# Kernel tuning notes

Hardware: AMD Instinct MI355X
Metric: run time of the kernel (lower is better)

The kernel has to match this reference:

```python
import jax, jax.numpy as jnp
import numpy as np

D_MODEL = 2048
B, L = 4, 2048


def _dwconv(x, w, b):
    # x: (B, D, L), w: (D, 1, 3), b: (D,). Causal depthwise conv (PyTorch pad=2 then [...,:L]).
    y = jax.lax.conv_general_dilated(
        x, w, window_strides=(1,), padding=[(2, 0)],
        feature_group_count=x.shape[1], dimension_numbers=("NCH", "OIH", "NCH"))
    return y + b[None, :, None]


def setup_inputs() -> dict:
    key = jax.random.key(0)
    ks = jax.random.split(key, 12)
    D = D_MODEL
    s = 0.02
    inp = {
        "u": jax.random.normal(ks[0], (B, L, D), jnp.float32),
        "Wq": jax.random.normal(ks[1], (D, D), jnp.float32) * s,
        "bq": jnp.zeros((D,), jnp.float32),
        "Wk": jax.random.normal(ks[2], (D, D), jnp.float32) * s,
        "bk": jnp.zeros((D,), jnp.float32),
        "Wv": jax.random.normal(ks[3], (D, D), jnp.float32) * s,
        "bv": jnp.zeros((D,), jnp.float32),
        "convq_w": jax.random.normal(ks[4], (D, 1, 3), jnp.float32) * 0.5,
        "convq_b": jnp.zeros((D,), jnp.float32),
        "convk_w": jax.random.normal(ks[5], (D, 1, 3), jnp.float32) * 0.5,
        "convk_b": jnp.zeros((D,), jnp.float32),
        "ssm_kernel": jax.random.normal(ks[6], (D, L), jnp.float32) * 0.01,  # H = d_model (head_dim=1)
        "D_skip": jax.random.normal(ks[7], (D,), jnp.float32),
        "Wo": jax.random.normal(ks[8], (D, D), jnp.float32) * s,
        "bo": jnp.zeros((D,), jnp.float32),
    }
    return inp


def reference(u, Wq, bq, Wk, bk, Wv, bv, convq_w, convq_b, convk_w, convk_b,
              ssm_kernel, D_skip, Wo, bo):
    # u: (B, L, H)  head_dim = 1 so H == d_model
    Lq = u.shape[1]
    fft_size = 2 * Lq  # L_kernel + L with l_max=None, rate=1

    # q/k/v projections (W @ u.T + b in torch == u @ W.T + b)
    q = jnp.einsum("blh,eh->ble", u, Wq) + bq
    k = jnp.einsum("blh,eh->ble", u, Wk) + bk
    v = jnp.einsum("blh,eh->ble", u, Wv) + bv
    q = jnp.transpose(q, (0, 2, 1))  # (B, H, L)
    k = jnp.transpose(k, (0, 2, 1))
    v = jnp.transpose(v, (0, 2, 1))

    # causal depthwise short convs
    q = _dwconv(q, convq_w, convq_b)
    k = _dwconv(k, convk_w, convk_b)

    # head_dim = 1: kv outer product collapses to elementwise product (B, H, L)
    kv = k * v

    # FFT long convolution: torch does rfft(kv)/n * rfft(kernel), irfft norm='forward'
    # which equals the standard unnormalized circular conv below.
    kv_f = jnp.fft.rfft(kv, n=fft_size)
    kernel_f = jnp.fft.rfft(ssm_kernel, n=fft_size)  # (H, F)
    y = jnp.fft.irfft(kv_f * kernel_f, n=fft_size)[..., :Lq]

    # D skip and q gating
    y = (y + kv * D_skip[None, :, None]) * q  # (B, H, L)

    # output projection
    y = jnp.transpose(y, (0, 2, 1))  # (B, L, H)
    return jnp.einsum("blh,eh->ble", y, Wo) + bo
```

## Files before the change

### kernel.cpp

```cpp
#include <hip/hip_runtime.h>
#include <cstdint>
#include <cstddef>

#define DD 2048
#define LL 2048
#define BB 4
#define MM (BB * LL)
#define NN 6144

typedef __bf16 bf16;
typedef __bf16 bf16x8 __attribute__((ext_vector_type(8)));
typedef __bf16 bf16x4 __attribute__((ext_vector_type(4)));
typedef __bf16 bf16x2 __attribute__((ext_vector_type(2)));
typedef float f32x4 __attribute__((ext_vector_type(4)));

__device__ __forceinline__ void gload16(const void* g, void* l) {
    __builtin_amdgcn_global_load_lds(
        (const __attribute__((address_space(1))) void*)g,
        (__attribute__((address_space(3))) void*)l, 16, 0, 0);
}

__global__ __launch_bounds__(256) void cvt_f32_bf16(const float* __restrict__ s,
                                                    bf16* __restrict__ d, int n8) {
    int i = blockIdx.x * 256 + threadIdx.x;
    if (i >= n8) return;
    const float4* sp = (const float4*)s + (size_t)i * 2;
    float4 a = sp[0], b = sp[1];
    bf16x8 o;
    o[0] = (bf16)a.x; o[1] = (bf16)a.y; o[2] = (bf16)a.z; o[3] = (bf16)a.w;
    o[4] = (bf16)b.x; o[5] = (bf16)b.y; o[6] = (bf16)b.z; o[7] = (bf16)b.w;
    *((bf16x8*)d + i) = o;
}

__global__ __launch_bounds__(256) void gemm_qkv(const bf16* __restrict__ A,
                                                const bf16* __restrict__ Bm,
                                                const float* __restrict__ bq,
                                                const float* __restrict__ bk,
                                                const float* __restrict__ bv,
                                                bf16* __restrict__ CtOut) {
    __shared__ bf16 lds[128 * 136];
    bf16* As = lds;
    bf16* Bs = lds + 4096;
    const int tid = threadIdx.x;
    const int m0 = blockIdx.x * 128, n0 = blockIdx.y * 128;
    const int sr = tid >> 2, sc = (tid & 3) << 3;
    const bf16* gA0 = A + (size_t)(m0 + sr) * DD + sc;
    const bf16* gA1 = A + (size_t)(m0 + 64 + sr) * DD + sc;
    const bf16* gB0 = Bm + (size_t)(n0 + sr) * DD + sc;
    const bf16* gB1 = Bm + (size_t)(n0 + 64 + sr) * DD + sc;
    bf16* lA0 = As + tid * 8;
    bf16* lA1 = As + 2048 + tid * 8;
    bf16* lB0 = Bs + tid * 8;
    bf16* lB1 = Bs + 2048 + tid * 8;

    const int wave = tid >> 6, lane = tid & 63;
    const int wm = (wave >> 1) << 6, wn = (wave & 1) << 6;
    const int fm = lane & 15, fg = lane >> 4;

    f32x4 acc[4][4];
#pragma unroll
    for (int i = 0; i < 4; i++)
#pragma unroll
        for (int j = 0; j < 4; j++) acc[i][j] = (f32x4){0.f, 0.f, 0.f, 0.f};

    for (int k0 = 0; k0 < DD; k0 += 32) {
        gload16(gA0, lA0);
        gload16(gA1, lA1);
        gload16(gB0, lB0);
        gload16(gB1, lB1);
        gA0 += 32; gA1 += 32; gB0 += 32; gB1 += 32;
        __syncthreads();

        bf16x8 af[4], bfr[4];
#pragma unroll
        for (int i = 0; i < 4; i++)
            af[i] = *(const bf16x8*)(As + (wm + i * 16 + fm) * 32 + fg * 8);
#pragma unroll
        for (int j = 0; j < 4; j++)
            bfr[j] = *(const bf16x8*)(Bs + (wn + j * 16 + fm) * 32 + fg * 8);
#pragma unroll
        for (int i = 0; i < 4; i++)
#pragma unroll
            for (int j = 0; j < 4; j++)
                acc[i][j] = __builtin_amdgcn_mfma_f32_16x16x32_bf16(
                    af[i], bfr[j], acc[i][j], 0, 0, 0);
        __syncthreads();
    }

    const float* bp = (n0 < 2048) ? bq : ((n0 < 4096) ? bk : bv);
    const int nb = n0 & 2047;
#pragma unroll
    for (int j = 0; j < 4; j++) {
        const int col = wn + j * 16 + fm;
        const float bvv = bp[nb + col];
#pragma unroll
        for (int i = 0; i < 4; i++) {
#pragma unroll
            for (int r = 0; r < 4; r++) {
                const int row = wm + i * 16 + fg * 4 + r;
                lds[col * 136 + row] = (bf16)(acc[i][j][r] + bvv);
            }
        }
    }
    __syncthreads();
    const int ccol = tid >> 4, chunk = tid & 15;
#pragma unroll
    for (int p = 0; p < 8; p++) {
        const int col = p * 16 + ccol;
        bf16x8 vv = *(const bf16x8*)&lds[col * 136 + chunk * 8];
        *(bf16x8*)(CtOut + (size_t)(n0 + col) * MM + m0 + chunk * 8) = vv;
    }
}

__global__ __launch_bounds__(256) void gemm_bt_f32(const bf16* __restrict__ A,
                                                   const bf16* __restrict__ Bm,
                                                   const float* __restrict__ bias,
                                                   float* __restrict__ C,
                                                   int Ndim, int Kdim) {
    __shared__ bf16 As[128 * 32];
    __shared__ bf16 Bs[128 * 32];
    const int tid = threadIdx.x;
    const int m0 = blockIdx.x * 128, n0 = blockIdx.y * 128;
    const int sr = tid >> 2, sc = (tid & 3) << 3;
    const bf16* gA0 = A + (size_t)(m0 + sr) * Kdim + sc;
    const bf16* gA1 = A + (size_t)(m0 + 64 + sr) * Kdim + sc;
    const bf16* gB0 = Bm + (size_t)(n0 + sr) * Kdim + sc;
    const bf16* gB1 = Bm + (size_t)(n0 + 64 + sr) * Kdim + sc;
    bf16* lA0 = As + tid * 8;
    bf16* lA1 = As + 2048 + tid * 8;
    bf16* lB0 = Bs + tid * 8;
    bf16* lB1 = Bs + 2048 + tid * 8;

    const int wave = tid >> 6, lane = tid & 63;
    const int wm = (wave >> 1) << 6, wn = (wave & 1) << 6;
    const int fm = lane & 15, fg = lane >> 4;

    f32x4 acc[4][4];
#pragma unroll
    for (int i = 0; i < 4; i++)
#pragma unroll
        for (int j = 0; j < 4; j++) acc[i][j] = (f32x4){0.f, 0.f, 0.f, 0.f};

    for (int k0 = 0; k0 < Kdim; k0 += 32) {
        gload16(gA0, lA0);
        gload16(gA1, lA1);
        gload16(gB0, lB0);
        gload16(gB1, lB1);
        gA0 += 32; gA1 += 32; gB0 += 32; gB1 += 32;
        __syncthreads();

        bf16x8 af[4], bfr[4];
#pragma unroll
        for (int i = 0; i < 4; i++)
            af[i] = *(const bf16x8*)(As + (wm + i * 16 + fm) * 32 + fg * 8);
#pragma unroll
        for (int j = 0; j < 4; j++)
            bfr[j] = *(const bf16x8*)(Bs + (wn + j * 16 + fm) * 32 + fg * 8);
#pragma unroll
        for (int i = 0; i < 4; i++)
#pragma unroll
            for (int j = 0; j < 4; j++)
                acc[i][j] = __builtin_amdgcn_mfma_f32_16x16x32_bf16(
                    af[i], bfr[j], acc[i][j], 0, 0, 0);
        __syncthreads();
    }

#pragma unroll
    for (int j = 0; j < 4; j++) {
        const int col = n0 + wn + j * 16 + fm;
        const float bv = bias[col];
#pragma unroll
        for (int i = 0; i < 4; i++) {
#pragma unroll
            for (int r = 0; r < 4; r++) {
                const int row = m0 + wm + i * 16 + fg * 4 + r;
                C[(size_t)row * Ndim + col] = acc[i][j][r] + bv;
            }
        }
    }
}

__global__ __launch_bounds__(256) void dwconv_kv2(
    const bf16* __restrict__ qkvT,
    const float* __restrict__ cqw, const float* __restrict__ cqb,
    const float* __restrict__ ckw, const float* __restrict__ ckb,
    bf16* __restrict__ qcT, bf16* __restrict__ kvT) {
    const int bid = blockIdx.x;
    const int b = bid >> 11, d = bid & (DD - 1);
    const int tid = threadIdx.x;
    const int l = tid * 8;

    const bf16* qR = qkvT + (size_t)d * MM + b * LL;
    const bf16* kR = qkvT + (size_t)(2048 + d) * MM + b * LL;
    const bf16* vR = qkvT + (size_t)(4096 + d) * MM + b * LL;

    const float q0 = cqw[d * 3], q1 = cqw[d * 3 + 1], q2 = cqw[d * 3 + 2];
    const float k0 = ckw[d * 3], k1 = ckw[d * 3 + 1], k2 = ckw[d * 3 + 2];
    const float qb = cqb[d], kb = ckb[d];

    bf16x8 qx = *(const bf16x8*)(qR + l);
    bf16x8 kx = *(const bf16x8*)(kR + l);
    bf16x8 vx = *(const bf16x8*)(vR + l);

    float xq[10], xk[10];
    xq[0] = 0.f; xq[1] = 0.f; xk[0] = 0.f; xk[1] = 0.f;
    if (l >= 2) {
        bf16x2 qh = *(const bf16x2*)(qR + l - 2);
        bf16x2 kh = *(const bf16x2*)(kR + l - 2);
        xq[0] = (float)qh[0]; xq[1] = (float)qh[1];
        xk[0] = (float)kh[0]; xk[1] = (float)kh[1];
    }
#pragma unroll
    for (int c = 0; c < 8; c++) { xq[c + 2] = (float)qx[c]; xk[c + 2] = (float)kx[c]; }

    bf16x8 oq, okv;
#pragma unroll
    for (int c = 0; c < 8; c++) {
        float qc = q0 * xq[c] + q1 * xq[c + 1] + q2 * xq[c + 2] + qb;
        float kc = k0 * xk[c] + k1 * xk[c + 1] + k2 * xk[c + 2] + kb;
        oq[c] = (bf16)qc;
        okv[c] = (bf16)(kc * (float)vx[c]);
    }
    const size_t o = ((size_t)b * DD + d) * LL + l;
    *(bf16x8*)(qcT + o) = oq;
    *(bf16x8*)(kvT + o) = okv;
}

__global__ __launch_bounds__(128, 2) void longconv_gate(
    const bf16* __restrict__ kvT, const bf16* __restrict__ qcT,
    const float* __restrict__ kern, const float* __restrict__ Dskip,
    bf16* __restrict__ ygT) {
    __shared__ bf16 kv_ls[4 * 2112];
    __shared__ float krev_f[2112];
    const int d = blockIdx.x;
    const int tid = threadIdx.x;

    {
        const int bb = tid >> 5, t32 = tid & 31;
#pragma unroll
        for (int c = 0; c < 8; ++c) {
            const int l = (c * 32 + t32) * 8;
            bf16x8 v = *(const bf16x8*)(kvT + ((size_t)bb * DD + d) * LL + l);
            *(bf16x8*)&kv_ls[2112 * bb + 48 + l] = v;
        }
        if (tid < 48) {
#pragma unroll
            for (int b2 = 0; b2 < 4; b2++) kv_ls[2112 * b2 + tid] = (bf16)0.f;
        } else if (tid < 64) {
#pragma unroll
            for (int b2 = 0; b2 < 4; b2++) kv_ls[2112 * b2 + 2048 + tid] = (bf16)0.f;
        }
    }
    {
        const float* kr = kern + (size_t)d * LL;
#pragma unroll
        for (int c = 0; c < 16; ++c) {
            const int x = c * 128 + tid;
            krev_f[x] = kr[2047 - x];
        }
        if (tid < 64) krev_f[2048 + tid] = 0.f;
    }
    __syncthreads();

    const int lane = tid & 63;
    const int w = __builtin_amdgcn_readfirstlane(tid >> 6);
    const int n = lane & 15, q = lane >> 4;
    const int b = n & 3, pp = n >> 2;
    const int cB = 2112 * b + 16 * pp + 8 * q;

    f32x4 acc[16];
#pragma unroll
    for (int s = 0; s < 16; s++) acc[s] = (f32x4){0.f, 0.f, 0.f, 0.f};

    for (int it = 0; it < 64; ++it) {
        const int as = 2031 - 32 * it - n + 8 * q;
        float af[8];
#pragma unroll
        for (int j = 0; j < 8; j++) af[j] = krev_f[as + j];
        bf16x8 a;
#pragma unroll
        for (int j = 0; j < 8; j++) a[j] = (bf16)af[j];

        const int bbase = cB + 64 * w + 32 - 32 * it;
#pragma unroll
        for (int h = 0; h < 2; ++h) {
            bf16x8 bfr[8];
#pragma unroll
            for (int s8 = 0; s8 < 8; s8++) {
                const int s = h * 8 + s8;
                if (it <= 4 * s + 2 * w + 1)
                    bfr[s8] = *(const bf16x8*)&kv_ls[bbase + 128 * s];
            }
#pragma unroll
            for (int s8 = 0; s8 < 8; s8++) {
                const int s = h * 8 + s8;
                if (it <= 4 * s + 2 * w + 1)
                    acc[s] = __builtin_amdgcn_mfma_f32_16x16x32_bf16(
                        a, bfr[s8], acc[s], 0, 0, 0);
            }
        }
    }

    const float dsk = Dskip[d];
#pragma unroll
    for (int s = 0; s < 16; s++) {
        const int i = 2 * s + w;
        const int l = 64 * i + 16 * pp + 4 * q;
        const size_t gb = ((size_t)b * DD + d) * LL + l;
        bf16x4 qc4 = *(const bf16x4*)&qcT[gb];
        bf16x4 kv4 = *(const bf16x4*)&kv_ls[2112 * b + 48 + l];
        bf16x4 o;
#pragma unroll
        for (int r = 0; r < 4; r++) {
            float val = (acc[s][r] + (float)kv4[r] * dsk) * (float)qc4[r];
            o[r] = (bf16)val;
        }
        *(bf16x4*)&ygT[gb] = o;
    }
}

__global__ __launch_bounds__(256) void transpose_dl(const bf16* __restrict__ src,
                                                    bf16* __restrict__ dst) {
    __shared__ bf16 ts[32][33];
    const int b = blockIdx.z;
    const int l0 = blockIdx.x * 32, d0 = blockIdx.y * 32;
    const int tid = threadIdx.x;
    const int c = tid & 31, r0 = tid >> 5;
#pragma unroll
    for (int p = 0; p < 4; p++) {
        int r = r0 + p * 8;
        ts[r][c] = src[((size_t)b * DD + d0 + r) * LL + l0 + c];
    }
    __syncthreads();
#pragma unroll
    for (int p = 0; p < 4; p++) {
        int r = r0 + p * 8;
        dst[((size_t)b * LL + l0 + r) * DD + d0 + c] = ts[c][r];
    }
}

extern "C" void kernel_launch(void* const* d_in, const int* in_sizes, int n_in,
                              void* d_out, int out_size, void* d_ws, size_t ws_size,
                              hipStream_t stream) {
    const float* u   = (const float*)d_in[0];
    const float* Wq  = (const float*)d_in[1];
    const float* bq  = (const float*)d_in[2];
    const float* Wk  = (const float*)d_in[3];
    const float* bk  = (const float*)d_in[4];
    const float* Wv  = (const float*)d_in[5];
    const float* bv  = (const float*)d_in[6];
    const float* cqw = (const float*)d_in[7];
    const float* cqb = (const float*)d_in[8];
    const float* ckw = (const float*)d_in[9];
    const float* ckb = (const float*)d_in[10];
    const float* ssm = (const float*)d_in[11];
    const float* Dsk = (const float*)d_in[12];
    const float* Wo  = (const float*)d_in[13];
    const float* bo  = (const float*)d_in[14];

    char* w = (char*)d_ws;
    bf16* u_bf    = (bf16*)(w);
    bf16* Wqkv_bf = (bf16*)(w + 33554432ull);
    bf16* Wo_bf   = (bf16*)(w + 58720256ull);
    bf16* qkvT    = (bf16*)(w + 67108864ull);
    bf16* qcT     = (bf16*)(w + 167772160ull);
    bf16* kvT     = (bf16*)(w + 201326592ull);

    cvt_f32_bf16<<<8192, 256, 0, stream>>>(u, u_bf, MM * DD / 8);
    cvt_f32_bf16<<<2048, 256, 0, stream>>>(Wq, Wqkv_bf, DD * DD / 8);
    cvt_f32_bf16<<<2048, 256, 0, stream>>>(Wk, Wqkv_bf + 4194304, DD * DD / 8);
    cvt_f32_bf16<<<2048, 256, 0, stream>>>(Wv, Wqkv_bf + 8388608, DD * DD / 8);
    cvt_f32_bf16<<<2048, 256, 0, stream>>>(Wo, Wo_bf, DD * DD / 8);

    dim3 gq(MM / 128, NN / 128);
    gemm_qkv<<<gq, 256, 0, stream>>>(u_bf, Wqkv_bf, bq, bk, bv, qkvT);

    dwconv_kv2<<<BB * DD, 256, 0, stream>>>(qkvT, cqw, cqb, ckw, ckb, qcT, kvT);

    bf16* ygT = u_bf;
    longconv_gate<<<DD, 128, 0, stream>>>(kvT, qcT, ssm, Dsk, ygT);

    bf16* ygTT = qkvT;
    dim3 gc(LL / 32, DD / 32, BB);
    transpose_dl<<<gc, 256, 0, stream>>>(ygT, ygTT);

    dim3 gg(MM / 128, DD / 128);
    gemm_bt_f32<<<gg, 256, 0, stream>>>(ygTT, Wo_bf, bo, (float*)d_out, DD, DD);
}
```

Measured before the change: 667.8 us.

## Rewrite both GEMMs as 256x256 double-buffered MFMA tiles with swizzled LDS

Replaces the 128x128 single-buffered GEMM kernels with a shared 256x256-tile, 512-thread main loop. It double-buffers LDS via async global_load_lds, staged in halves interleaved with MFMA groups, and uses XOR-swizzled LDS addressing to avoid bank conflicts. It also sets wave priority around MFMA bursts and remaps block IDs for L2 locality. The aim is more data reuse per load and hiding global-load latency, at the cost of 128KB LDS per block and heavy register use, which limits occupancy.

```diff
diff --git a/kernel.cpp b/kernel.cpp
--- a/kernel.cpp
+++ b/kernel.cpp
@@ -32,149 +32,184 @@
     *((bf16x8*)d + i) = o;
 }
 
-__global__ __launch_bounds__(256) void gemm_qkv(const bf16* __restrict__ A,
-                                                const bf16* __restrict__ Bm,
-                                                const float* __restrict__ bq,
-                                                const float* __restrict__ bk,
-                                                const float* __restrict__ bv,
-                                                bf16* __restrict__ CtOut) {
-    __shared__ bf16 lds[128 * 136];
-    bf16* As = lds;
-    bf16* Bs = lds + 4096;
-    const int tid = threadIdx.x;
-    const int m0 = blockIdx.x * 128, n0 = blockIdx.y * 128;
-    const int sr = tid >> 2, sc = (tid & 3) << 3;
-    const bf16* gA0 = A + (size_t)(m0 + sr) * DD + sc;
-    const bf16* gA1 = A + (size_t)(m0 + 64 + sr) * DD + sc;
-    const bf16* gB0 = Bm + (size_t)(n0 + sr) * DD + sc;
-    const bf16* gB1 = Bm + (size_t)(n0 + 64 + sr) * DD + sc;
-    bf16* lA0 = As + tid * 8;
-    bf16* lA1 = As + 2048 + tid * 8;
-    bf16* lB0 = Bs + tid * 8;
-    bf16* lB1 = Bs + 2048 + tid * 8;
-
+__device__ __forceinline__ void stage_half(const bf16* g, bf16* l, size_t rstep, int tid) {
+    gload16(g, l + tid * 8);
+    gload16(g + rstep, l + 4096 + tid * 8);
+}
+
+#define MFMA16(J0, J1)                                                         \
+    __builtin_amdgcn_s_setprio(1);                                             \
+    _Pragma("unroll") for (int i = 0; i < 8; i++)                              \
+        acc[i][J0] = __builtin_amdgcn_mfma_f32_16x16x32_bf16(af[i], bq[J0],    \
+                                                             acc[i][J0], 0, 0, 0); \
+    _Pragma("unroll") for (int i = 0; i < 8; i++)                              \
+        acc[i][J1] = __builtin_amdgcn_mfma_f32_16x16x32_bf16(af[i], bq[J1],    \
+                                                             acc[i][J1], 0, 0, 0); \
+    __builtin_amdgcn_s_setprio(0);
+
+template <int NT>
+__device__ __forceinline__ void mma256_loop(const bf16* gA, const bf16* gB,
+                                            int Kdim, bf16* lds,
+                                            f32x4 (&acc)[8][4]) {
+    const int tid = threadIdx.x;
     const int wave = tid >> 6, lane = tid & 63;
-    const int wm = (wave >> 1) << 6, wn = (wave & 1) << 6;
+    const int wm = wave >> 2, wn = wave & 3;
     const int fm = lane & 15, fg = lane >> 4;
-
-    f32x4 acc[4][4];
-#pragma unroll
-    for (int i = 0; i < 4; i++)
+    const size_t rstep = (size_t)128 * Kdim;
+    const int koff = ((fg ^ ((fm >> 1) & 3)) << 3);
+    const int aoff = (wm * 128 + fm) * 32 + koff;
+    const int boff = (wn * 64 + fm) * 32 + koff;
+
+    bf16* const A0 = lds;
+    bf16* const B0 = lds + 32768;
+
+#pragma unroll
+    for (int i = 0; i < 8; i++)
 #pragma unroll
         for (int j = 0; j < 4; j++) acc[i][j] = (f32x4){0.f, 0.f, 0.f, 0.f};
 
-    for (int k0 = 0; k0 < DD; k0 += 32) {
-        gload16(gA0, lA0);
-        gload16(gA1, lA1);
-        gload16(gB0, lB0);
-        gload16(gB1, lB1);
-        gA0 += 32; gA1 += 32; gB0 += 32; gB1 += 32;
-        __syncthreads();
-
-        bf16x8 af[4], bfr[4];
-#pragma unroll
-        for (int i = 0; i < 4; i++)
-            af[i] = *(const bf16x8*)(As + (wm + i * 16 + fm) * 32 + fg * 8);
-#pragma unroll
-        for (int j = 0; j < 4; j++)
-            bfr[j] = *(const bf16x8*)(Bs + (wn + j * 16 + fm) * 32 + fg * 8);
-#pragma unroll
-        for (int i = 0; i < 4; i++)
-#pragma unroll
-            for (int j = 0; j < 4; j++)
-                acc[i][j] = __builtin_amdgcn_mfma_f32_16x16x32_bf16(
-                    af[i], bfr[j], acc[i][j], 0, 0, 0);
-        __syncthreads();
-    }
-
-    const float* bp = (n0 < 2048) ? bq : ((n0 < 4096) ? bk : bv);
+    stage_half(gA, A0, rstep, tid);
+    stage_half(gB, B0, rstep, tid);
+    stage_half(gA + 32, A0 + 8192, rstep, tid);
+    stage_half(gB + 32, B0 + 8192, rstep, tid);
+
+    bf16x8 af[8], bq[4];
+
+    for (int t = 0; t < NT; ++t) {
+        const int c = t & 1;
+        bf16* const Ac = A0 + c * 16384;
+        bf16* const Bc = B0 + c * 16384;
+        bf16* const An = A0 + (c ^ 1) * 16384;
+        bf16* const Bn = B0 + (c ^ 1) * 16384;
+        const bf16* a1 = gA + (t + 1) * 64;
+        const bf16* b1 = gB + (t + 1) * 64;
+        const bool st = (t + 1 < NT);
+
+        asm volatile("s_waitcnt vmcnt(4)" ::: "memory");
+        __builtin_amdgcn_s_barrier();
+        if (st) stage_half(a1, An, rstep, tid);
+#pragma unroll
+        for (int i = 0; i < 8; i++) af[i] = *(const bf16x8*)(Ac + aoff + i * 512);
+        bq[0] = *(const bf16x8*)(Bc + boff);
+        bq[1] = *(const bf16x8*)(Bc + boff + 512);
+        __builtin_amdgcn_s_barrier();
+        asm volatile("s_waitcnt lgkmcnt(0)" ::: "memory");
+        MFMA16(0, 1)
+
+        __builtin_amdgcn_s_barrier();
+        if (st) stage_half(b1, Bn, rstep, tid);
+        bq[2] = *(const bf16x8*)(Bc + boff + 1024);
+        bq[3] = *(const bf16x8*)(Bc + boff + 1536);
+        __builtin_amdgcn_s_barrier();
+        asm volatile("s_waitcnt lgkmcnt(0)" ::: "memory");
+        MFMA16(2, 3)
+
+        if (st) { asm volatile("s_waitcnt vmcnt(4)" ::: "memory"); }
+        else    { asm volatile("s_waitcnt vmcnt(0)" ::: "memory"); }
+        __builtin_amdgcn_s_barrier();
+        if (st) stage_half(a1 + 32, An + 8192, rstep, tid);
+#pragma unroll
+        for (int i = 0; i < 8; i++) af[i] = *(const bf16x8*)(Ac + 8192 + aoff + i * 512);
+        bq[0] = *(const bf16x8*)(Bc + 8192 + boff);
+        bq[1] = *(const bf16x8*)(Bc + 8192 + boff + 512);
+        __builtin_amdgcn_s_barrier();
+        asm volatile("s_waitcnt lgkmcnt(0)" ::: "memory");
+        MFMA16(0, 1)
+
+        __builtin_amdgcn_s_barrier();
+        if (st) stage_half(b1 + 32, Bn + 8192, rstep, tid);
+        bq[2] = *(const bf16x8*)(Bc + 8192 + boff + 1024);
+        bq[3] = *(const bf16x8*)(Bc + 8192 + boff + 1536);
+        __builtin_amdgcn_s_barrier();
+        asm volatile("s_waitcnt lgkmcnt(0)" ::: "memory");
+        MFMA16(2, 3)
+    }
+}
+
+__global__ __launch_bounds__(512, 2) void gemm_qkv(const bf16* __restrict__ A,
+                                                   const bf16* __restrict__ Bm,
+                                                   const float* __restrict__ bqp,
+                                                   const float* __restrict__ bkp,
+                                                   const float* __restrict__ bvp,
+                                                   bf16* __restrict__ CtOut) {
+    __shared__ bf16 lds[65536];
+    const int id = blockIdx.x;
+    const int wg = (id & 7) * 96 + (id >> 3);
+    const int m0 = (wg & 31) << 8;
+    const int n0 = (wg >> 5) << 8;
+
+    const int tid = threadIdx.x;
+    const int wave = tid >> 6, lane = tid & 63;
+    const int srow = tid >> 2;
+    const int skx = (((lane & 3) ^ ((lane >> 3) & 3)) << 3);
+    const bf16* gA = A + (size_t)(m0 + srow) * DD + skx;
+    const bf16* gB = Bm + (size_t)(n0 + srow) * DD + skx;
+
+    f32x4 acc[8][4];
+    mma256_loop<DD / 64>(gA, gB, DD, lds, acc);
+
+    __syncthreads();
+    const int wm = wave >> 2, wn = wave & 3;
+    const int fm = lane & 15, fg = lane >> 4;
+    const float* bp = (n0 < 2048) ? bqp : ((n0 < 4096) ? bkp : bvp);
     const int nb = n0 & 2047;
 #pragma unroll
     for (int j = 0; j < 4; j++) {
-        const int col = wn + j * 16 + fm;
+        const int col = wn * 64 + j * 16 + fm;
         const float bvv = bp[nb + col];
-#pragma unroll
-        for (int i = 0; i < 4; i++) {
+        const int csw = (col & 7) << 3;
+#pragma unroll
+        for (int i = 0; i < 8; i++) {
+            const int row = (wm * 128 + i * 16 + fg * 4) ^ csw;
+            bf16x4 o;
+#pragma unroll
+            for (int r = 0; r < 4; r++) o[r] = (bf16)(acc[i][j][r] + bvv);
+            *(bf16x4*)&lds[col * 256 + row] = o;
+        }
+    }
+    __syncthreads();
+    const int ccol = tid >> 5, chunk = tid & 31;
+#pragma unroll
+    for (int p = 0; p < 16; p++) {
+        const int col = p * 16 + ccol;
+        bf16x8 vv = *(const bf16x8*)&lds[col * 256 + ((chunk * 8) ^ ((col & 7) << 3))];
+        *(bf16x8*)(CtOut + (size_t)(n0 + col) * MM + m0 + chunk * 8) = vv;
+    }
+}
+
+__global__ __launch_bounds__(512, 2) void gemm_bt_f32(const bf16* __restrict__ A,
+                                                      const bf16* __restrict__ Bm,
+                                                      const float* __restrict__ bias,
+                                                      float* __restrict__ C,
+                                                      int Ndim, int Kdim) {
+    __shared__ bf16 lds[65536];
+    const int id = blockIdx.x;
+    const int wg = (id & 7) * (gridDim.x >> 3) + (id >> 3);
+    const int m0 = (wg & 31) << 8;
+    const int n0 = (wg >> 5) << 8;
+
+    const int tid = threadIdx.x;
+    const int wave = tid >> 6, lane = tid & 63;
+    const int srow = tid >> 2;
+    const int skx = (((lane & 3) ^ ((lane >> 3) & 3)) << 3);
+    const bf16* gA = A + (size_t)(m0 + srow) * Kdim + skx;
+    const bf16* gB = Bm + (size_t)(n0 + srow) * Kdim + skx;
+
+    f32x4 acc[8][4];
+    mma256_loop<DD / 64>(gA, gB, Kdim, lds, acc);
+
+    const int wm = wave >> 2, wn = wave & 3;
+    const int fm = lane & 15, fg = lane >> 4;
+#pragma unroll
+    for (int j = 0; j < 4; j++) {
+        const int col = n0 + wn * 64 + j * 16 + fm;
+        const float bvv = bias[col];
+#pragma unroll
+        for (int i = 0; i < 8; i++) {
 #pragma unroll
             for (int r = 0; r < 4; r++) {
-                const int row = wm + i * 16 + fg * 4 + r;
-                lds[col * 136 + row] = (bf16)(acc[i][j][r] + bvv);
-            }
-        }
-    }
-    __syncthreads();
-    const int ccol = tid >> 4, chunk = tid & 15;
-#pragma unroll
-    for (int p = 0; p < 8; p++) {
-        const int col = p * 16 + ccol;
-        bf16x8 vv = *(const bf16x8*)&lds[col * 136 + chunk * 8];
-        *(bf16x8*)(CtOut + (size_t)(n0 + col) * MM + m0 + chunk * 8) = vv;
-    }
-}
-
-__global__ __launch_bounds__(256) void gemm_bt_f32(const bf16* __restrict__ A,
-                                                   const bf16* __restrict__ Bm,
-                                                   const float* __restrict__ bias,
-                                                   float* __restrict__ C,
-                                                   int Ndim, int Kdim) {
-    __shared__ bf16 As[128 * 32];
-    __shared__ bf16 Bs[128 * 32];
-    const int tid = threadIdx.x;
-    const int m0 = blockIdx.x * 128, n0 = blockIdx.y * 128;
-    const int sr = tid >> 2, sc = (tid & 3) << 3;
-    const bf16* gA0 = A + (size_t)(m0 + sr) * Kdim + sc;
-    const bf16* gA1 = A + (size_t)(m0 + 64 + sr) * Kdim + sc;
-    const bf16* gB0 = Bm + (size_t)(n0 + sr) * Kdim + sc;
-    const bf16* gB1 = Bm + (size_t)(n0 + 64 + sr) * Kdim + sc;
-    bf16* lA0 = As + tid * 8;
-    bf16* lA1 = As + 2048 + tid * 8;
-    bf16* lB0 = Bs + tid * 8;
-    bf16* lB1 = Bs + 2048 + tid * 8;
-
-    const int wave = tid >> 6, lane = tid & 63;
-    const int wm = (wave >> 1) << 6, wn = (wave & 1) << 6;
-    const int fm = lane & 15, fg = lane >> 4;
-
-    f32x4 acc[4][4];
-#pragma unroll
-    for (int i = 0; i < 4; i++)
-#pragma unroll
-        for (int j = 0; j < 4; j++) acc[i][j] = (f32x4){0.f, 0.f, 0.f, 0.f};
-
-    for (int k0 = 0; k0 < Kdim; k0 += 32) {
-        gload16(gA0, lA0);
-        gload16(gA1, lA1);
-        gload16(gB0, lB0);
-        gload16(gB1, lB1);
-        gA0 += 32; gA1 += 32; gB0 += 32; gB1 += 32;
-        __syncthreads();
-
-        bf16x8 af[4], bfr[4];
-#pragma unroll
-        for (int i = 0; i < 4; i++)
-            af[i] = *(const bf16x8*)(As + (wm + i * 16 + fm) * 32 + fg * 8);
-#pragma unroll
-        for (int j = 0; j < 4; j++)
-            bfr[j] = *(const bf16x8*)(Bs + (wn + j * 16 + fm) * 32 + fg * 8);
-#pragma unroll
-        for (int i = 0; i < 4; i++)
-#pragma unroll
-            for (int j = 0; j < 4; j++)
-                acc[i][j] = __builtin_amdgcn_mfma_f32_16x16x32_bf16(
-                    af[i], bfr[j], acc[i][j], 0, 0, 0);
-        __syncthreads();
-    }
-
-#pragma unroll
-    for (int j = 0; j < 4; j++) {
-        const int col = n0 + wn + j * 16 + fm;
-        const float bv = bias[col];
-#pragma unroll
-        for (int i = 0; i < 4; i++) {
-#pragma unroll
-            for (int r = 0; r < 4; r++) {
-                const int row = m0 + wm + i * 16 + fg * 4 + r;
-                C[(size_t)row * Ndim + col] = acc[i][j][r] + bv;
+                const int row = m0 + wm * 128 + i * 16 + fg * 4 + r;
+                C[(size_t)row * Ndim + col] = acc[i][j][r] + bvv;
             }
         }
     }
@@ -372,8 +407,7 @@
     cvt_f32_bf16<<<2048, 256, 0, stream>>>(Wv, Wqkv_bf + 8388608, DD * DD / 8);
     cvt_f32_bf16<<<2048, 256, 0, stream>>>(Wo, Wo_bf, DD * DD / 8);
 
-    dim3 gq(MM / 128, NN / 128);
-    gemm_qkv<<<gq, 256, 0, stream>>>(u_bf, Wqkv_bf, bq, bk, bv, qkvT);
+    gemm_qkv<<<(MM / 256) * (NN / 256), 512, 0, stream>>>(u_bf, Wqkv_bf, bq, bk, bv, qkvT);
 
     dwconv_kv2<<<BB * DD, 256, 0, stream>>>(qkvT, cqw, cqb, ckw, ckb, qcT, kvT);
 
@@ -384,6 +418,6 @@
     dim3 gc(LL / 32, DD / 32, BB);
     transpose_dl<<<gc, 256, 0, stream>>>(ygT, ygTT);
 
-    dim3 gg(MM / 128, DD / 128);
-    gemm_bt_f32<<<gg, 256, 0, stream>>>(ygTT, Wo_bf, bo, (float*)d_out, DD, DD);
-}
+    gemm_bt_f32<<<(MM / 256) * (DD / 256), 512, 0, stream>>>(ygTT, Wo_bf, bo,
+                                                             (float*)d_out, DD, DD);
+}
```

Result: faster. 586.6 us (-12.2%).
